# Optimization experiments

Measured on AMD Instinct MI355X. Metric: run time of the kernel, lower is better.

The kernel has to match this reference:

```python
import jax, jax.numpy as jnp
import numpy as np

NUM_LAYER, BS, NUM_HEADS, INPUT_LEN, ENC_LEN = 4, 2, 16, 1024, 588
HID = 256
LN_EPS = 1e-5


def _ln(x, g, b):
    mu = jnp.mean(x, axis=-1, keepdims=True)
    var = jnp.mean((x - mu) ** 2, axis=-1, keepdims=True)
    return (x - mu) / jnp.sqrt(var + LN_EPS) * g + b


def _mlp(x, Ws, bs, gs, betas):
    # 3-layer LayerNorm -> Linear (+GELU except last)
    n = len(Ws)
    for i in range(n):
        x = _ln(x, gs[i], betas[i])
        x = x @ Ws[i] + bs[i]
        if i < n - 1:
            x = jax.nn.gelu(x, approximate=False)  # torch F.gelu default = exact
    return x


def setup_inputs() -> dict:
    key = jax.random.key(0)
    ks = jax.random.split(key, 24)
    s = 0.02
    dims = [(ENC_LEN, HID), (HID, HID), (HID, 4)]
    inp = {
        "heatmap": jax.random.normal(ks[0], (NUM_LAYER, BS, NUM_HEADS, INPUT_LEN, ENC_LEN), jnp.float32),
        "attention_valid_mask": jnp.ones((BS, INPUT_LEN), jnp.float32),
        "W_head": jax.random.normal(ks[1], (NUM_LAYER * NUM_HEADS, 1), jnp.float32) * s,
        "b_head": jnp.zeros((1,), jnp.float32),
        "W_keep": jax.random.normal(ks[2], (ENC_LEN, 1), jnp.float32) * s,
        "b_keep": jnp.zeros((1,), jnp.float32),
    }
    for br in (1, 2):
        for i, (di, do) in enumerate(dims):
            inp[f"W{br}_{i}"] = jax.random.normal(ks[3 + br * 4 + i], (di, do), jnp.float32) * s
            inp[f"b{br}_{i}"] = jnp.zeros((do,), jnp.float32)
    for i, d in enumerate([ENC_LEN, HID, HID]):
        inp[f"g{i}"] = jnp.ones((d,), jnp.float32)
        inp[f"beta{i}"] = jnp.zeros((d,), jnp.float32)
    return inp


def reference(heatmap, attention_valid_mask, W_head, b_head, W_keep, b_keep,
              W1_0, b1_0, W1_1, b1_1, W1_2, b1_2,
              W2_0, b2_0, W2_1, b2_1, W2_2, b2_2,
              g0, beta0, g1, beta1, g2, beta2):
    num_layer, bs, num_heads, input_len, enc_len = heatmap.shape
    # [L,B,H,T,E] -> [B,T,E,L*H]
    hm = jnp.transpose(heatmap, (1, 3, 4, 0, 2)).reshape(bs, input_len, enc_len, num_layer * num_heads)
    x = (hm @ W_head + b_head)[..., 0]            # [B,T,E]
    x = x.reshape(bs * input_len, enc_len)        # [B*T, 588]
    logits_keep_row = (x @ W_keep + b_keep)[:, 0]  # [B*T]

    gs, betas = [g0, g1, g2], [beta0, beta1, beta2]
    out1 = _mlp(x, [W1_0, W1_1, W1_2], [b1_0, b1_1, b1_2], gs, betas)
    out2 = _mlp(x, [W2_0, W2_1, W2_2], [b2_0, b2_1, b2_2], gs, betas)
    keep = (jax.nn.sigmoid(logits_keep_row) > 0.5)[:, None]  # keep_row_thres = 0.5
    out = jnp.where(keep, out1, out2)             # gather/compute/scatter == select

    out = jax.nn.sigmoid(out.reshape(bs, input_len, 4))
    # input_len != 4095, so the mask-shift branch is skipped
    out = out * attention_valid_mask[:, :, None]
    x1, y1, w, h = out[:, :, 0], out[:, :, 1], out[:, :, 2], out[:, :, 3]
    return (x1, y1, x1 + w, y1 + h, logits_keep_row)
```

## Files before the change

kernel.cpp:

```cpp
#include <hip/hip_runtime.h>
#include <hip/hip_bf16.h>
#include <math.h>

#define NLAYER 4
#define BSZ 2
#define NHEADS 16
#define ILEN 1024
#define ELEN 588
#define HID 256
#define NROWS (BSZ * ILEN)
#define NCH (NLAYER * NHEADS)
#define S_H ((size_t)(ILEN) * ELEN)
#define S_B ((size_t)NHEADS * S_H)
#define S_L ((size_t)BSZ * S_B)

__device__ __forceinline__ float gelu_exact(float x) {
    return 0.5f * x * (1.0f + erff(x * 0.70710678118654752440f));
}
__device__ __forceinline__ float sigmoidf(float x) {
    return 1.0f / (1.0f + expf(-x));
}
__device__ __forceinline__ float wave_sum(float v) {
    #pragma unroll
    for (int m = 1; m < 64; m <<= 1) v += __shfl_xor(v, m);
    return v;
}

__global__ __launch_bounds__(256) void k_reduce_ln0(
    const float* __restrict__ hm, const float* __restrict__ Wh,
    const float* __restrict__ bh, const float* __restrict__ Wk,
    const float* __restrict__ bk, const float* __restrict__ g0,
    const float* __restrict__ be0, float* __restrict__ y,
    float* __restrict__ keepf, float* __restrict__ out_logits)
{
    const int row = blockIdx.x;
    const int b = row >> 10;
    const int i = row & 1023;
    const int tid = threadIdx.x;

    __shared__ float s_wh[NCH];
    __shared__ float s_wk[ELEN];
    __shared__ float s_red[12];
    __shared__ float s_bcast[2];

    if (tid < NCH) s_wh[tid] = Wh[tid];
    for (int e = tid; e < ELEN; e += 256) s_wk[e] = Wk[e];
    __syncthreads();

    const int f4 = tid;
    float4 acc = make_float4(0.f, 0.f, 0.f, 0.f);

    if (f4 < 147) {
        const float* rowbase = hm + (size_t)b * S_B + (size_t)i * ELEN + (size_t)(f4 * 4);
        #pragma unroll 8
        for (int ch = 0; ch < NCH; ++ch) {
            const size_t off = (size_t)(ch >> 4) * S_L + (size_t)(ch & 15) * S_H;
            const float4 v = *(const float4*)(rowbase + off);
            const float w = s_wh[ch];
            acc.x += v.x * w; acc.y += v.y * w;
            acc.z += v.z * w; acc.w += v.w * w;
        }
        const float bhv = bh[0];
        acc.x += bhv; acc.y += bhv; acc.z += bhv; acc.w += bhv;
    }

    float sx = 0.f, sxx = 0.f, sk = 0.f;
    if (f4 < 147) {
        sx  = acc.x + acc.y + acc.z + acc.w;
        sxx = acc.x * acc.x + acc.y * acc.y + acc.z * acc.z + acc.w * acc.w;
        const float4 wk = *(const float4*)&s_wk[f4 * 4];
        sk  = acc.x * wk.x + acc.y * wk.y + acc.z * wk.z + acc.w * wk.w;
    }
    #pragma unroll
    for (int off = 32; off; off >>= 1) {
        sx  += __shfl_down(sx, off);
        sxx += __shfl_down(sxx, off);
        sk  += __shfl_down(sk, off);
    }
    const int wid = tid >> 6, lane = tid & 63;
    if (lane == 0) { s_red[wid] = sx; s_red[4 + wid] = sxx; s_red[8 + wid] = sk; }
    __syncthreads();
    if (tid == 0) {
        sx  = s_red[0] + s_red[1] + s_red[2] + s_red[3];
        sxx = s_red[4] + s_red[5] + s_red[6] + s_red[7];
        sk  = s_red[8] + s_red[9] + s_red[10] + s_red[11];
        const float mu   = sx * (1.0f / ELEN);
        const float var  = sxx * (1.0f / ELEN) - mu * mu;
        const float rstd = rsqrtf(var + 1e-5f);
        const float logit = sk + bk[0];
        s_bcast[0] = mu; s_bcast[1] = rstd;
        out_logits[row] = logit;
        keepf[row] = (logit > 0.f) ? 1.f : 0.f;
    }
    __syncthreads();
    if (f4 < 147) {
        const float mu = s_bcast[0], rstd = s_bcast[1];
        const float4 gv = *(const float4*)&g0[f4 * 4];
        const float4 bv = *(const float4*)&be0[f4 * 4];
        float4 o;
        o.x = (acc.x - mu) * rstd * gv.x + bv.x;
        o.y = (acc.y - mu) * rstd * gv.y + bv.y;
        o.z = (acc.z - mu) * rstd * gv.z + bv.z;
        o.w = (acc.w - mu) * rstd * gv.w + bv.w;
        *(float4*)&y[(size_t)row * ELEN + f4 * 4] = o;
    }
}

__global__ __launch_bounds__(256) void k_mlp0(
    const float* __restrict__ y,
    const float* __restrict__ W10, const float* __restrict__ b10,
    const float* __restrict__ W20, const float* __restrict__ b20,
    const float* __restrict__ g1, const float* __restrict__ be1,
    float* __restrict__ h1n, float* __restrict__ h2n)
{
    __shared__ float y_lds[8][ELEN];
    const int tid  = threadIdx.x;
    const int row0 = blockIdx.x * 8;

    for (int fi = tid; fi < 8 * 147; fi += 256) {
        const int r = fi / 147, t = fi % 147;
        *(float4*)&y_lds[r][t * 4] =
            *(const float4*)&y[(size_t)(row0 + r) * ELEN + t * 4];
    }
    __syncthreads();

    const int lane = tid & 63;
    const int rg   = tid >> 6;
    const int col  = lane * 4;
    const int lr0  = rg * 2, lr1 = lr0 + 1;

    const float4 gg  = *(const float4*)&g1[col];
    const float4 bb1 = *(const float4*)&be1[col];

    #pragma unroll
    for (int br = 0; br < 2; ++br) {
        const float* W  = br ? W20 : W10;
        const float* bb = br ? b20 : b10;
        float4 a0 = make_float4(0.f, 0.f, 0.f, 0.f);
        float4 a1 = make_float4(0.f, 0.f, 0.f, 0.f);

        for (int e = 0; e < ELEN; e += 2) {
            const float2 ya = *(const float2*)&y_lds[lr0][e];
            const float2 yb = *(const float2*)&y_lds[lr1][e];
            const float4 w0 = *(const float4*)&W[(size_t)e * HID + col];
            const float4 w1 = *(const float4*)&W[(size_t)(e + 1) * HID + col];
            a0.x += ya.x * w0.x + ya.y * w1.x;
            a0.y += ya.x * w0.y + ya.y * w1.y;
            a0.z += ya.x * w0.z + ya.y * w1.z;
            a0.w += ya.x * w0.w + ya.y * w1.w;
            a1.x += yb.x * w0.x + yb.y * w1.x;
            a1.y += yb.x * w0.y + yb.y * w1.y;
            a1.z += yb.x * w0.z + yb.y * w1.z;
            a1.w += yb.x * w0.w + yb.y * w1.w;
        }

        const float4 bv = *(const float4*)&bb[col];
        float* hdst = br ? h2n : h1n;

        #pragma unroll
        for (int r = 0; r < 2; ++r) {
            float4 v = r ? a1 : a0;
            v.x = gelu_exact(v.x + bv.x);
            v.y = gelu_exact(v.y + bv.y);
            v.z = gelu_exact(v.z + bv.z);
            v.w = gelu_exact(v.w + bv.w);
            float s1 = v.x + v.y + v.z + v.w;
            float s2 = v.x * v.x + v.y * v.y + v.z * v.z + v.w * v.w;
            s1 = wave_sum(s1);
            s2 = wave_sum(s2);
            const float mu   = s1 * (1.0f / HID);
            const float rstd = rsqrtf(s2 * (1.0f / HID) - mu * mu + 1e-5f);
            float4 o;
            o.x = (v.x - mu) * rstd * gg.x + bb1.x;
            o.y = (v.y - mu) * rstd * gg.y + bb1.y;
            o.z = (v.z - mu) * rstd * gg.z + bb1.z;
            o.w = (v.w - mu) * rstd * gg.w + bb1.w;
            const int grow = row0 + (r ? lr1 : lr0);
            *(float4*)&hdst[(size_t)grow * HID + col] = o;
        }
    }
}

__global__ __launch_bounds__(256) void k_mlp12(
    const float* __restrict__ h1n, const float* __restrict__ h2n,
    const float* __restrict__ W11, const float* __restrict__ b11,
    const float* __restrict__ W21, const float* __restrict__ b21,
    const float* __restrict__ W12, const float* __restrict__ b12,
    const float* __restrict__ W22, const float* __restrict__ b22,
    const float* __restrict__ g2, const float* __restrict__ be2,
    const float* __restrict__ keepf, const float* __restrict__ mask,
    float* __restrict__ dout)
{
    __shared__ float h_lds[8][HID];
    const int tid  = threadIdx.x;
    const int row0 = blockIdx.x * 8;
    const int lane = tid & 63;
    const int rg   = tid >> 6;
    const int col  = lane * 4;
    const int lr0  = rg * 2, lr1 = lr0 + 1;

    const float4 gg  = *(const float4*)&g2[col];
    const float4 bb2 = *(const float4*)&be2[col];

    float res[2][2][4];

    #pragma unroll
    for (int br = 0; br < 2; ++br) {
        const float* hsrc = br ? h2n : h1n;
        __syncthreads();
        for (int fi = tid; fi < 8 * 64; fi += 256) {
            const int r = fi >> 6, t = fi & 63;
            *(float4*)&h_lds[r][t * 4] =
                *(const float4*)&hsrc[(size_t)(row0 + r) * HID + t * 4];
        }
        __syncthreads();

        const float* W  = br ? W21 : W11;
        const float* bb = br ? b21 : b11;
        float4 a0 = make_float4(0.f, 0.f, 0.f, 0.f);
        float4 a1 = make_float4(0.f, 0.f, 0.f, 0.f);

        for (int e = 0; e < HID; e += 2) {
            const float2 ya = *(const float2*)&h_lds[lr0][e];
            const float2 yb = *(const float2*)&h_lds[lr1][e];
            const float4 w0 = *(const float4*)&W[(size_t)e * HID + col];
            const float4 w1 = *(const float4*)&W[(size_t)(e + 1) * HID + col];
            a0.x += ya.x * w0.x + ya.y * w1.x;
            a0.y += ya.x * w0.y + ya.y * w1.y;
            a0.z += ya.x * w0.z + ya.y * w1.z;
            a0.w += ya.x * w0.w + ya.y * w1.w;
            a1.x += yb.x * w0.x + yb.y * w1.x;
            a1.y += yb.x * w0.y + yb.y * w1.y;
            a1.z += yb.x * w0.z + yb.y * w1.z;
            a1.w += yb.x * w0.w + yb.y * w1.w;
        }

        const float4 bv = *(const float4*)&bb[col];
        const float* W2 = br ? W22 : W12;
        const float* b2 = br ? b22 : b12;

        #pragma unroll
        for (int r = 0; r < 2; ++r) {
            float4 v = r ? a1 : a0;
            v.x = gelu_exact(v.x + bv.x);
            v.y = gelu_exact(v.y + bv.y);
            v.z = gelu_exact(v.z + bv.z);
            v.w = gelu_exact(v.w + bv.w);
            float s1 = v.x + v.y + v.z + v.w;
            float s2 = v.x * v.x + v.y * v.y + v.z * v.z + v.w * v.w;
            s1 = wave_sum(s1);
            s2 = wave_sum(s2);
            const float mu   = s1 * (1.0f / HID);
            const float rstd = rsqrtf(s2 * (1.0f / HID) - mu * mu + 1e-5f);
            float zn[4];
            zn[0] = (v.x - mu) * rstd * gg.x + bb2.x;
            zn[1] = (v.y - mu) * rstd * gg.y + bb2.y;
            zn[2] = (v.z - mu) * rstd * gg.z + bb2.z;
            zn[3] = (v.w - mu) * rstd * gg.w + bb2.w;

            float p[4] = {0.f, 0.f, 0.f, 0.f};
            #pragma unroll
            for (int k = 0; k < 4; ++k) {
                const float4 w4 = *(const float4*)&W2[(size_t)(col + k) * 4];
                p[0] += zn[k] * w4.x;
                p[1] += zn[k] * w4.y;
                p[2] += zn[k] * w4.z;
                p[3] += zn[k] * w4.w;
            }
            #pragma unroll
            for (int c = 0; c < 4; ++c) {
                p[c] = wave_sum(p[c]);
                res[br][r][c] = p[c] + b2[c];
            }
        }
    }

    if (lane == 0) {
        #pragma unroll
        for (int r = 0; r < 2; ++r) {
            const int grow = row0 + lr0 + r;
            const float kf = keepf[grow];
            const float m  = mask[grow];
            const float* sel = (kf > 0.5f) ? res[0][r] : res[1][r];
            const float x1 = sigmoidf(sel[0]) * m;
            const float y1 = sigmoidf(sel[1]) * m;
            const float w  = sigmoidf(sel[2]) * m;
            const float h  = sigmoidf(sel[3]) * m;
            dout[grow]            = x1;
            dout[NROWS + grow]    = y1;
            dout[2 * NROWS + grow] = x1 + w;
            dout[3 * NROWS + grow] = y1 + h;
        }
    }
}

extern "C" void kernel_launch(void* const* d_in, const int* in_sizes, int n_in,
                              void* d_out, int out_size, void* d_ws, size_t ws_size,
                              hipStream_t stream)
{
    const float* hm   = (const float*)d_in[0];
    const float* mask = (const float*)d_in[1];
    const float* Wh   = (const float*)d_in[2];
    const float* bh   = (const float*)d_in[3];
    const float* Wk   = (const float*)d_in[4];
    const float* bk   = (const float*)d_in[5];
    const float* W10  = (const float*)d_in[6];
    const float* b10  = (const float*)d_in[7];
    const float* W11  = (const float*)d_in[8];
    const float* b11  = (const float*)d_in[9];
    const float* W12  = (const float*)d_in[10];
    const float* b12  = (const float*)d_in[11];
    const float* W20  = (const float*)d_in[12];
    const float* b20  = (const float*)d_in[13];
    const float* W21  = (const float*)d_in[14];
    const float* b21  = (const float*)d_in[15];
    const float* W22  = (const float*)d_in[16];
    const float* b22  = (const float*)d_in[17];
    const float* g0   = (const float*)d_in[18];
    const float* be0  = (const float*)d_in[19];
    const float* g1   = (const float*)d_in[20];
    const float* be1  = (const float*)d_in[21];
    const float* g2   = (const float*)d_in[22];
    const float* be2  = (const float*)d_in[23];

    float* ws    = (float*)d_ws;
    float* y     = ws;
    float* h1n   = y + (size_t)NROWS * ELEN;
    float* h2n   = h1n + (size_t)NROWS * HID;
    float* keepf = h2n + (size_t)NROWS * HID;
    float* dout  = (float*)d_out;

    k_reduce_ln0<<<NROWS, 256, 0, stream>>>(hm, Wh, bh, Wk, bk, g0, be0,
                                            y, keepf, dout + 4 * NROWS);
    k_mlp0<<<NROWS / 8, 256, 0, stream>>>(y, W10, b10, W20, b20, g1, be1,
                                          h1n, h2n);
    k_mlp12<<<NROWS / 8, 256, 0, stream>>>(h1n, h2n, W11, b11, W21, b21,
                                           W12, b12, W22, b22, g2, be2,
                                           keepf, mask, dout);
}
```

Before: 621.6 us.

## Fuse MLP kernels into one and use nontemporal loads for heatmap reduction

Merges the two MLP kernels into a single 512-thread kernel. Each wave now handles one row end to end, and the hidden activations stay in LDS instead of round-tripping through global workspace. The keep flag is dropped, and the logit is re-read from the output buffer instead. The heatmap reduction switches to nontemporal vector loads with deeper unrolling to stream the large input. The risk is less weight reuse per wave, since one row per wave instead of two doubles the global and L2 weight reads per row.

```diff
diff --git a/kernel.cpp b/kernel.cpp
--- a/kernel.cpp
+++ b/kernel.cpp
@@ -14,6 +14,8 @@
 #define S_B ((size_t)NHEADS * S_H)
 #define S_L ((size_t)BSZ * S_B)
 
+typedef float f32x4 __attribute__((ext_vector_type(4)));
+
 __device__ __forceinline__ float gelu_exact(float x) {
     return 0.5f * x * (1.0f + erff(x * 0.70710678118654752440f));
 }
@@ -31,7 +33,7 @@
     const float* __restrict__ bh, const float* __restrict__ Wk,
     const float* __restrict__ bk, const float* __restrict__ g0,
     const float* __restrict__ be0, float* __restrict__ y,
-    float* __restrict__ keepf, float* __restrict__ out_logits)
+    float* __restrict__ out_logits)
 {
     const int row = blockIdx.x;
     const int b = row >> 10;
@@ -48,17 +50,15 @@
     __syncthreads();
 
     const int f4 = tid;
-    float4 acc = make_float4(0.f, 0.f, 0.f, 0.f);
+    f32x4 acc = {0.f, 0.f, 0.f, 0.f};
 
     if (f4 < 147) {
         const float* rowbase = hm + (size_t)b * S_B + (size_t)i * ELEN + (size_t)(f4 * 4);
-        #pragma unroll 8
+        #pragma unroll 16
         for (int ch = 0; ch < NCH; ++ch) {
             const size_t off = (size_t)(ch >> 4) * S_L + (size_t)(ch & 15) * S_H;
-            const float4 v = *(const float4*)(rowbase + off);
-            const float w = s_wh[ch];
-            acc.x += v.x * w; acc.y += v.y * w;
-            acc.z += v.z * w; acc.w += v.w * w;
+            const f32x4 v = __builtin_nontemporal_load((const f32x4*)(rowbase + off));
+            acc += v * s_wh[ch];
         }
         const float bhv = bh[0];
         acc.x += bhv; acc.y += bhv; acc.z += bhv; acc.w += bhv;
@@ -87,10 +87,8 @@
         const float mu   = sx * (1.0f / ELEN);
         const float var  = sxx * (1.0f / ELEN) - mu * mu;
         const float rstd = rsqrtf(var + 1e-5f);
-        const float logit = sk + bk[0];
         s_bcast[0] = mu; s_bcast[1] = rstd;
-        out_logits[row] = logit;
-        keepf[row] = (logit > 0.f) ? 1.f : 0.f;
+        out_logits[row] = sk + bk[0];
     }
     __syncthreads();
     if (f4 < 147) {
@@ -106,191 +104,139 @@
     }
 }
 
-__global__ __launch_bounds__(256) void k_mlp0(
+__global__ __launch_bounds__(512) void k_mlp_fused(
     const float* __restrict__ y,
     const float* __restrict__ W10, const float* __restrict__ b10,
+    const float* __restrict__ W11, const float* __restrict__ b11,
+    const float* __restrict__ W12, const float* __restrict__ b12,
     const float* __restrict__ W20, const float* __restrict__ b20,
+    const float* __restrict__ W21, const float* __restrict__ b21,
+    const float* __restrict__ W22, const float* __restrict__ b22,
     const float* __restrict__ g1, const float* __restrict__ be1,
-    float* __restrict__ h1n, float* __restrict__ h2n)
+    const float* __restrict__ g2, const float* __restrict__ be2,
+    const float* __restrict__ mask, float* __restrict__ dout)
 {
     __shared__ float y_lds[8][ELEN];
+    __shared__ float h_lds[8][HID];
+
     const int tid  = threadIdx.x;
     const int row0 = blockIdx.x * 8;
 
-    for (int fi = tid; fi < 8 * 147; fi += 256) {
+    for (int fi = tid; fi < 8 * 147; fi += 512) {
         const int r = fi / 147, t = fi % 147;
         *(float4*)&y_lds[r][t * 4] =
             *(const float4*)&y[(size_t)(row0 + r) * ELEN + t * 4];
     }
     __syncthreads();
 
+    const int w    = tid >> 6;
     const int lane = tid & 63;
-    const int rg   = tid >> 6;
     const int col  = lane * 4;
-    const int lr0  = rg * 2, lr1 = lr0 + 1;
-
-    const float4 gg  = *(const float4*)&g1[col];
-    const float4 bb1 = *(const float4*)&be1[col];
+    const int grow = row0 + w;
+
+    const float4 gg1 = *(const float4*)&g1[col];
+    const float4 be1v = *(const float4*)&be1[col];
+    const float4 gg2 = *(const float4*)&g2[col];
+    const float4 be2v = *(const float4*)&be2[col];
+
+    float res[2][4];
 
     #pragma unroll
     for (int br = 0; br < 2; ++br) {
-        const float* W  = br ? W20 : W10;
-        const float* bb = br ? b20 : b10;
-        float4 a0 = make_float4(0.f, 0.f, 0.f, 0.f);
-        float4 a1 = make_float4(0.f, 0.f, 0.f, 0.f);
-
-        for (int e = 0; e < ELEN; e += 2) {
-            const float2 ya = *(const float2*)&y_lds[lr0][e];
-            const float2 yb = *(const float2*)&y_lds[lr1][e];
-            const float4 w0 = *(const float4*)&W[(size_t)e * HID + col];
-            const float4 w1 = *(const float4*)&W[(size_t)(e + 1) * HID + col];
-            a0.x += ya.x * w0.x + ya.y * w1.x;
-            a0.y += ya.x * w0.y + ya.y * w1.y;
-            a0.z += ya.x * w0.z + ya.y * w1.z;
-            a0.w += ya.x * w0.w + ya.y * w1.w;
-            a1.x += yb.x * w0.x + yb.y * w1.x;
-            a1.y += yb.x * w0.y + yb.y * w1.y;
-            a1.z += yb.x * w0.z + yb.y * w1.z;
-            a1.w += yb.x * w0.w + yb.y * w1.w;
-        }
-
-        const float4 bv = *(const float4*)&bb[col];
-        float* hdst = br ? h2n : h1n;
-
-        #pragma unroll
-        for (int r = 0; r < 2; ++r) {
-            float4 v = r ? a1 : a0;
-            v.x = gelu_exact(v.x + bv.x);
-            v.y = gelu_exact(v.y + bv.y);
-            v.z = gelu_exact(v.z + bv.z);
-            v.w = gelu_exact(v.w + bv.w);
-            float s1 = v.x + v.y + v.z + v.w;
-            float s2 = v.x * v.x + v.y * v.y + v.z * v.z + v.w * v.w;
-            s1 = wave_sum(s1);
-            s2 = wave_sum(s2);
+        const float* W0  = br ? W20 : W10;
+        const float* bb0 = br ? b20 : b10;
+        const float* W1  = br ? W21 : W11;
+        const float* bb1 = br ? b21 : b11;
+        const float* W2  = br ? W22 : W12;
+        const float* bb2 = br ? b22 : b12;
+
+        float4 a = make_float4(0.f, 0.f, 0.f, 0.f);
+        for (int e = 0; e < ELEN; e += 4) {
+            const float4 ya = *(const float4*)&y_lds[w][e];
+            const float4 w0 = *(const float4*)&W0[(size_t)(e + 0) * HID + col];
+            const float4 w1 = *(const float4*)&W0[(size_t)(e + 1) * HID + col];
+            const float4 w2 = *(const float4*)&W0[(size_t)(e + 2) * HID + col];
+            const float4 w3 = *(const float4*)&W0[(size_t)(e + 3) * HID + col];
+            a.x += ya.x * w0.x + ya.y * w1.x + ya.z * w2.x + ya.w * w3.x;
+            a.y += ya.x * w0.y + ya.y * w1.y + ya.z * w2.y + ya.w * w3.y;
+            a.z += ya.x * w0.z + ya.y * w1.z + ya.z * w2.z + ya.w * w3.z;
+            a.w += ya.x * w0.w + ya.y * w1.w + ya.z * w2.w + ya.w * w3.w;
+        }
+        {
+            const float4 bv = *(const float4*)&bb0[col];
+            a.x = gelu_exact(a.x + bv.x);
+            a.y = gelu_exact(a.y + bv.y);
+            a.z = gelu_exact(a.z + bv.z);
+            a.w = gelu_exact(a.w + bv.w);
+        }
+        {
+            float s1 = wave_sum(a.x + a.y + a.z + a.w);
+            float s2 = wave_sum(a.x * a.x + a.y * a.y + a.z * a.z + a.w * a.w);
             const float mu   = s1 * (1.0f / HID);
             const float rstd = rsqrtf(s2 * (1.0f / HID) - mu * mu + 1e-5f);
             float4 o;
-            o.x = (v.x - mu) * rstd * gg.x + bb1.x;
-            o.y = (v.y - mu) * rstd * gg.y + bb1.y;
-            o.z = (v.z - mu) * rstd * gg.z + bb1.z;
-            o.w = (v.w - mu) * rstd * gg.w + bb1.w;
-            const int grow = row0 + (r ? lr1 : lr0);
-            *(float4*)&hdst[(size_t)grow * HID + col] = o;
-        }
-    }
-}
-
-__global__ __launch_bounds__(256) void k_mlp12(
-    const float* __restrict__ h1n, const float* __restrict__ h2n,
-    const float* __restrict__ W11, const float* __restrict__ b11,
-    const float* __restrict__ W21, const float* __restrict__ b21,
-    const float* __restrict__ W12, const float* __restrict__ b12,
-    const float* __restrict__ W22, const float* __restrict__ b22,
-    const float* __restrict__ g2, const float* __restrict__ be2,
-    const float* __restrict__ keepf, const float* __restrict__ mask,
-    float* __restrict__ dout)
-{
-    __shared__ float h_lds[8][HID];
-    const int tid  = threadIdx.x;
-    const int row0 = blockIdx.x * 8;
-    const int lane = tid & 63;
-    const int rg   = tid >> 6;
-    const int col  = lane * 4;
-    const int lr0  = rg * 2, lr1 = lr0 + 1;
-
-    const float4 gg  = *(const float4*)&g2[col];
-    const float4 bb2 = *(const float4*)&be2[col];
-
-    float res[2][2][4];
-
-    #pragma unroll
-    for (int br = 0; br < 2; ++br) {
-        const float* hsrc = br ? h2n : h1n;
-        __syncthreads();
-        for (int fi = tid; fi < 8 * 64; fi += 256) {
-            const int r = fi >> 6, t = fi & 63;
-            *(float4*)&h_lds[r][t * 4] =
-                *(const float4*)&hsrc[(size_t)(row0 + r) * HID + t * 4];
-        }
-        __syncthreads();
-
-        const float* W  = br ? W21 : W11;
-        const float* bb = br ? b21 : b11;
-        float4 a0 = make_float4(0.f, 0.f, 0.f, 0.f);
-        float4 a1 = make_float4(0.f, 0.f, 0.f, 0.f);
-
-        for (int e = 0; e < HID; e += 2) {
-            const float2 ya = *(const float2*)&h_lds[lr0][e];
-            const float2 yb = *(const float2*)&h_lds[lr1][e];
-            const float4 w0 = *(const float4*)&W[(size_t)e * HID + col];
-            const float4 w1 = *(const float4*)&W[(size_t)(e + 1) * HID + col];
-            a0.x += ya.x * w0.x + ya.y * w1.x;
-            a0.y += ya.x * w0.y + ya.y * w1.y;
-            a0.z += ya.x * w0.z + ya.y * w1.z;
-            a0.w += ya.x * w0.w + ya.y * w1.w;
-            a1.x += yb.x * w0.x + yb.y * w1.x;
-            a1.y += yb.x * w0.y + yb.y * w1.y;
-            a1.z += yb.x * w0.z + yb.y * w1.z;
-            a1.w += yb.x * w0.w + yb.y * w1.w;
-        }
-
-        const float4 bv = *(const float4*)&bb[col];
-        const float* W2 = br ? W22 : W12;
-        const float* b2 = br ? b22 : b12;
-
-        #pragma unroll
-        for (int r = 0; r < 2; ++r) {
-            float4 v = r ? a1 : a0;
-            v.x = gelu_exact(v.x + bv.x);
-            v.y = gelu_exact(v.y + bv.y);
-            v.z = gelu_exact(v.z + bv.z);
-            v.w = gelu_exact(v.w + bv.w);
-            float s1 = v.x + v.y + v.z + v.w;
-            float s2 = v.x * v.x + v.y * v.y + v.z * v.z + v.w * v.w;
-            s1 = wave_sum(s1);
-            s2 = wave_sum(s2);
+            o.x = (a.x - mu) * rstd * gg1.x + be1v.x;
+            o.y = (a.y - mu) * rstd * gg1.y + be1v.y;
+            o.z = (a.z - mu) * rstd * gg1.z + be1v.z;
+            o.w = (a.w - mu) * rstd * gg1.w + be1v.w;
+            *(float4*)&h_lds[w][col] = o;
+        }
+        float4 c = make_float4(0.f, 0.f, 0.f, 0.f);
+        for (int e = 0; e < HID; e += 4) {
+            const float4 ha = *(const float4*)&h_lds[w][e];
+            const float4 w0 = *(const float4*)&W1[(size_t)(e + 0) * HID + col];
+            const float4 w1 = *(const float4*)&W1[(size_t)(e + 1) * HID + col];
+            const float4 w2 = *(const float4*)&W1[(size_t)(e + 2) * HID + col];
+            const float4 w3 = *(const float4*)&W1[(size_t)(e + 3) * HID + col];
+            c.x += ha.x * w0.x + ha.y * w1.x + ha.z * w2.x + ha.w * w3.x;
+            c.y += ha.x * w0.y + ha.y * w1.y + ha.z * w2.y + ha.w * w3.y;
+            c.z += ha.x * w0.z + ha.y * w1.z + ha.z * w2.z + ha.w * w3.z;
+            c.w += ha.x * w0.w + ha.y * w1.w + ha.z * w2.w + ha.w * w3.w;
+        }
+        {
+            const float4 bv = *(const float4*)&bb1[col];
+            c.x = gelu_exact(c.x + bv.x);
+            c.y = gelu_exact(c.y + bv.y);
+            c.z = gelu_exact(c.z + bv.z);
+            c.w = gelu_exact(c.w + bv.w);
+        }
+        float zn[4];
+        {
+            float s1 = wave_sum(c.x + c.y + c.z + c.w);
+            float s2 = wave_sum(c.x * c.x + c.y * c.y + c.z * c.z + c.w * c.w);
             const float mu   = s1 * (1.0f / HID);
             const float rstd = rsqrtf(s2 * (1.0f / HID) - mu * mu + 1e-5f);
-            float zn[4];
-            zn[0] = (v.x - mu) * rstd * gg.x + bb2.x;
-            zn[1] = (v.y - mu) * rstd * gg.y + bb2.y;
-            zn[2] = (v.z - mu) * rstd * gg.z + bb2.z;
-            zn[3] = (v.w - mu) * rstd * gg.w + bb2.w;
-
-            float p[4] = {0.f, 0.f, 0.f, 0.f};
-            #pragma unroll
-            for (int k = 0; k < 4; ++k) {
-                const float4 w4 = *(const float4*)&W2[(size_t)(col + k) * 4];
-                p[0] += zn[k] * w4.x;
-                p[1] += zn[k] * w4.y;
-                p[2] += zn[k] * w4.z;
-                p[3] += zn[k] * w4.w;
-            }
-            #pragma unroll
-            for (int c = 0; c < 4; ++c) {
-                p[c] = wave_sum(p[c]);
-                res[br][r][c] = p[c] + b2[c];
-            }
-        }
+            zn[0] = (c.x - mu) * rstd * gg2.x + be2v.x;
+            zn[1] = (c.y - mu) * rstd * gg2.y + be2v.y;
+            zn[2] = (c.z - mu) * rstd * gg2.z + be2v.z;
+            zn[3] = (c.w - mu) * rstd * gg2.w + be2v.w;
+        }
+        float p[4] = {0.f, 0.f, 0.f, 0.f};
+        #pragma unroll
+        for (int k = 0; k < 4; ++k) {
+            const float4 w4 = *(const float4*)&W2[(size_t)(col + k) * 4];
+            p[0] += zn[k] * w4.x;
+            p[1] += zn[k] * w4.y;
+            p[2] += zn[k] * w4.z;
+            p[3] += zn[k] * w4.w;
+        }
+        #pragma unroll
+        for (int cc = 0; cc < 4; ++cc)
+            res[br][cc] = wave_sum(p[cc]) + bb2[cc];
     }
 
     if (lane == 0) {
-        #pragma unroll
-        for (int r = 0; r < 2; ++r) {
-            const int grow = row0 + lr0 + r;
-            const float kf = keepf[grow];
-            const float m  = mask[grow];
-            const float* sel = (kf > 0.5f) ? res[0][r] : res[1][r];
-            const float x1 = sigmoidf(sel[0]) * m;
-            const float y1 = sigmoidf(sel[1]) * m;
-            const float w  = sigmoidf(sel[2]) * m;
-            const float h  = sigmoidf(sel[3]) * m;
-            dout[grow]            = x1;
-            dout[NROWS + grow]    = y1;
-            dout[2 * NROWS + grow] = x1 + w;
-            dout[3 * NROWS + grow] = y1 + h;
-        }
+        const float logit = dout[4 * NROWS + grow];
+        const float m = mask[grow];
+        const float* sel = (logit > 0.f) ? res[0] : res[1];
+        const float x1 = sigmoidf(sel[0]) * m;
+        const float y1 = sigmoidf(sel[1]) * m;
+        const float ww = sigmoidf(sel[2]) * m;
+        const float hh = sigmoidf(sel[3]) * m;
+        dout[grow]             = x1;
+        dout[NROWS + grow]     = y1;
+        dout[2 * NROWS + grow] = x1 + ww;
+        dout[3 * NROWS + grow] = y1 + hh;
     }
 }
 
@@ -323,18 +269,13 @@
     const float* g2   = (const float*)d_in[22];
     const float* be2  = (const float*)d_in[23];
 
-    float* ws    = (float*)d_ws;
-    float* y     = ws;
-    float* h1n   = y + (size_t)NROWS * ELEN;
-    float* h2n   = h1n + (size_t)NROWS * HID;
-    float* keepf = h2n + (size_t)NROWS * HID;
-    float* dout  = (float*)d_out;
+    float* ws   = (float*)d_ws;
+    float* y    = ws;
+    float* dout = (float*)d_out;
 
     k_reduce_ln0<<<NROWS, 256, 0, stream>>>(hm, Wh, bh, Wk, bk, g0, be0,
-                                            y, keepf, dout + 4 * NROWS);
-    k_mlp0<<<NROWS / 8, 256, 0, stream>>>(y, W10, b10, W20, b20, g1, be1,
-                                          h1n, h2n);
-    k_mlp12<<<NROWS / 8, 256, 0, stream>>>(h1n, h2n, W11, b11, W21, b21,
-                                           W12, b12, W22, b22, g2, be2,
-                                           keepf, mask, dout);
-}
+                                            y, dout + 4 * NROWS);
+    k_mlp_fused<<<NROWS / 8, 512, 0, stream>>>(y, W10, b10, W11, b11, W12, b12,
+                                               W20, b20, W21, b21, W22, b22,
+                                               g1, be1, g2, be2, mask, dout);
+}
```

Measured after the change: 547.7 us. 11.9% less time.
